# Optimization experiments

Measured on AMD Instinct MI355X. Metric: run time of the kernel, lower is better.

Reference implementation:

```python
import jax, jax.numpy as jnp
import numpy as np

B, S, H = 64, 2048, 512
NEG = -1e9

def setup_inputs() -> dict:
    key = jax.random.key(0)
    k1, k2, k3, k4, k5 = jax.random.split(key, 5)
    encoder_outputs = jax.random.normal(k1, (B, S, H), dtype=jnp.float32)
    mask = jax.random.randint(k2, (B, S), 0, 2).astype(bool)
    W = jax.random.normal(k3, (H, H), dtype=jnp.float32) / np.sqrt(H)
    b = jnp.zeros((H,), dtype=jnp.float32)
    v = jax.random.normal(k4, (H,), dtype=jnp.float32)  # context_vector
    return {"encoder_outputs": encoder_outputs, "mask": mask, "W": W, "b": b, "v": v}

def reference(encoder_outputs, mask, W, b, v):
    # u = tanh(x @ W^T + b): [B,S,H]
    u = jnp.tanh(jnp.einsum('bsh,oh->bso', encoder_outputs, W) + b)
    scores = jnp.einsum('bsh,h->bs', u, v)                 # [B,S]
    scores = jnp.where(mask, scores, NEG)
    attn_weights = jax.nn.softmax(scores, axis=1)          # [B,S]
    weighted_output = jnp.einsum('bsh,bs->bh', encoder_outputs, attn_weights)
    return weighted_output, attn_weights
```

## Files before the change

kernel.cpp:

```cpp
#include <hip/hip_runtime.h>
#include <hip/hip_fp16.h>
#include <stdint.h>

#define NEG_ (-1e9f)

typedef _Float16 f16x8 __attribute__((ext_vector_type(8)));
typedef float    f32x4 __attribute__((ext_vector_type(4)));

__device__ __forceinline__ float fast_tanh(float x) {
  float e = __expf(2.0f * x);
  return (e - 1.0f) * __builtin_amdgcn_rcpf(e + 1.0f);
}

__global__ __launch_bounds__(256) void k0_cvt_w(const float* __restrict__ W,
                                                __half* __restrict__ Wws) {
  int g = blockIdx.x * 256 + threadIdx.x;
  int lane = g & 63;
  int seg  = g >> 6;
  int io = seg & 3, ks = (seg >> 2) & 15, w = seg >> 6;
  int o = w * 64 + io * 16 + (lane & 15);
  int k = ks * 32 + (lane >> 4) * 8;
  const float2* src = (const float2*)(W + (size_t)o * 512 + k);
  __half2 h[4];
#pragma unroll
  for (int j = 0; j < 4; ++j) { float2 f = src[j]; h[j] = __floats2half2_rn(f.x, f.y); }
  uint4 u;
  u.x = *(uint32_t*)&h[0]; u.y = *(uint32_t*)&h[1];
  u.z = *(uint32_t*)&h[2]; u.w = *(uint32_t*)&h[3];
  *(uint4*)(Wws + (size_t)seg * 512 + (size_t)lane * 8) = u;
}

__global__ __launch_bounds__(512, 4) void k1_scores(
    const float* __restrict__ enc, const int* __restrict__ msk,
    const float* __restrict__ bias, const float* __restrict__ ctx,
    const __half* __restrict__ Wws, float* __restrict__ scores) {
  __shared__ __align__(16) __half Xl[64 * 512];

  const int t = threadIdx.x;
  const int w = t >> 6;
  const int lane = t & 63;
  const int quad = lane >> 4;
  const int l15 = lane & 15;
  const size_t mtile = blockIdx.x;

  {
    const float4* Xg = (const float4*)(enc + mtile * (size_t)(64 * 512));
#pragma unroll
    for (int j = 0; j < 8; ++j) {
      int g = j * 512 + t;
      int s = g >> 6, c = g & 63;
      float4 x0 = Xg[s * 128 + 2 * c];
      float4 x1 = Xg[s * 128 + 2 * c + 1];
      __half2 h0 = __floats2half2_rn(x0.x, x0.y);
      __half2 h1 = __floats2half2_rn(x0.z, x0.w);
      __half2 h2 = __floats2half2_rn(x1.x, x1.y);
      __half2 h3 = __floats2half2_rn(x1.z, x1.w);
      uint4 u;
      u.x = *(uint32_t*)&h0; u.y = *(uint32_t*)&h1;
      u.z = *(uint32_t*)&h2; u.w = *(uint32_t*)&h3;
      int pc = c ^ (s & 7);
      *(uint4*)&Xl[s * 512 + pc * 8] = u;
    }
  }
  __syncthreads();

  f16x8 abuf[3][4];
  auto aload = [&](int slot, int ks) {
    const f16x8* sp = (const f16x8*)(Wws +
        ((size_t)(w * 64 + ks * 4) * 512) + (size_t)lane * 8);
#pragma unroll
    for (int io = 0; io < 4; ++io) abuf[slot][io] = sp[io * 64];
  };
  aload(0, 0);
  aload(1, 1);

  f32x4 acc[4][4];
#pragma unroll
  for (int io = 0; io < 4; ++io)
#pragma unroll
    for (int is = 0; is < 4; ++is) acc[io][is] = (f32x4){0.f, 0.f, 0.f, 0.f};

#pragma unroll
  for (int ks = 0; ks < 16; ++ks) {
    if (ks + 2 < 16) aload((ks + 2) % 3, ks + 2);
    const f16x8* acur = abuf[ks % 3];
#pragma unroll
    for (int is = 0; is < 4; ++is) {
      int s = is * 16 + l15;
      const f16x8 bf = *(const f16x8*)&Xl[s * 512 + (((ks * 4 + quad) ^ (s & 7)) << 3)];
#pragma unroll
      for (int io = 0; io < 4; ++io)
        acc[io][is] = __builtin_amdgcn_mfma_f32_16x16x32_f16(acur[io], bf, acc[io][is], 0, 0, 0);
    }
  }

  float ps[4] = {0.f, 0.f, 0.f, 0.f};
#pragma unroll
  for (int io = 0; io < 4; ++io) {
    int ob = w * 64 + io * 16 + quad * 4;
    float4 b4 = *(const float4*)(bias + ob);
    float4 v4 = *(const float4*)(ctx + ob);
#pragma unroll
    for (int is = 0; is < 4; ++is) {
      const f32x4 a = acc[io][is];
      ps[is] += fast_tanh(a[0] + b4.x) * v4.x + fast_tanh(a[1] + b4.y) * v4.y +
                fast_tanh(a[2] + b4.z) * v4.z + fast_tanh(a[3] + b4.w) * v4.w;
    }
  }
#pragma unroll
  for (int is = 0; is < 4; ++is) {
    ps[is] += __shfl_xor(ps[is], 16, 64);
    ps[is] += __shfl_xor(ps[is], 32, 64);
  }

  __syncthreads();
  float* sred = (float*)&Xl[0];
  if (lane < 16) {
#pragma unroll
    for (int is = 0; is < 4; ++is) sred[w * 64 + is * 16 + lane] = ps[is];
  }
  __syncthreads();
  if (t < 64) {
    float sc = 0.f;
#pragma unroll
    for (int k = 0; k < 8; ++k) sc += sred[k * 64 + t];
    size_t row = mtile * 64 + t;
    scores[row] = msk[row] ? sc : NEG_;
  }
}

__global__ __launch_bounds__(256) void k2_softmax(float* __restrict__ attn) {
  const int b = blockIdx.x, t = threadIdx.x;
  float* row = attn + (size_t)b * 2048;
  float v[8];
  float mx = -3.4e38f;
#pragma unroll
  for (int i = 0; i < 8; ++i) { v[i] = row[t + 256 * i]; mx = fmaxf(mx, v[i]); }
#pragma unroll
  for (int off = 32; off >= 1; off >>= 1) mx = fmaxf(mx, __shfl_xor(mx, off, 64));
  __shared__ float r1[4], r2[4];
  int w = t >> 6, lane = t & 63;
  if (lane == 0) r1[w] = mx;
  __syncthreads();
  mx = fmaxf(fmaxf(r1[0], r1[1]), fmaxf(r1[2], r1[3]));
  float sum = 0.f;
#pragma unroll
  for (int i = 0; i < 8; ++i) { v[i] = __expf(v[i] - mx); sum += v[i]; }
#pragma unroll
  for (int off = 32; off >= 1; off >>= 1) sum += __shfl_xor(sum, off, 64);
  if (lane == 0) r2[w] = sum;
  __syncthreads();
  sum = r2[0] + r2[1] + r2[2] + r2[3];
  float inv = 1.0f / sum;
#pragma unroll
  for (int i = 0; i < 8; ++i) row[t + 256 * i] = v[i] * inv;
}

__global__ __launch_bounds__(256) void k3_wsum(const float* __restrict__ enc,
                                               const float* __restrict__ attn,
                                               float* __restrict__ out0) {
  const int bb = blockIdx.x >> 5, sc = blockIdx.x & 31, t = threadIdx.x;
  const int r = t >> 7;
  const int c = t & 127;
  __shared__ float a_s[64];
  __shared__ __align__(16) float4 part[128];
  if (t < 64) a_s[t] = attn[(size_t)bb * 2048 + sc * 64 + t];
  __syncthreads();
  const float4* Xg = (const float4*)(enc + ((size_t)bb * 2048 + (size_t)sc * 64) * 512);
  float4 acc = {0.f, 0.f, 0.f, 0.f};
#pragma unroll 8
  for (int s = r; s < 64; s += 2) {
    float a = a_s[s];
    float4 x = Xg[(size_t)s * 128 + c];
    acc.x = fmaf(a, x.x, acc.x);
    acc.y = fmaf(a, x.y, acc.y);
    acc.z = fmaf(a, x.z, acc.z);
    acc.w = fmaf(a, x.w, acc.w);
  }
  if (r) part[c] = acc;
  __syncthreads();
  if (!r) {
    float4 o = part[c];
    float* op = out0 + (size_t)bb * 512 + c * 4;
    atomicAdd(op + 0, acc.x + o.x);
    atomicAdd(op + 1, acc.y + o.y);
    atomicAdd(op + 2, acc.z + o.z);
    atomicAdd(op + 3, acc.w + o.w);
  }
}

extern "C" void kernel_launch(void* const* d_in, const int* in_sizes, int n_in,
                              void* d_out, int out_size, void* d_ws, size_t ws_size,
                              hipStream_t stream) {
  (void)in_sizes; (void)n_in; (void)out_size; (void)ws_size;
  const float* enc  = (const float*)d_in[0];
  const int*   msk  = (const int*)d_in[1];
  const float* W    = (const float*)d_in[2];
  const float* bias = (const float*)d_in[3];
  const float* ctx  = (const float*)d_in[4];
  float* out0 = (float*)d_out;
  float* attn = out0 + 64 * 512;
  __half* Wws = (__half*)d_ws;

  hipMemsetAsync(out0, 0, 64 * 512 * sizeof(float), stream);
  k0_cvt_w<<<128, 256, 0, stream>>>(W, Wws);
  k1_scores<<<2048, 512, 0, stream>>>(enc, msk, bias, ctx, Wws, attn);
  k2_softmax<<<64, 256, 0, stream>>>(attn);
  k3_wsum<<<2048, 256, 0, stream>>>(enc, attn, out0);
}
```

Baseline: 517.1 us.

## Fuse softmax-weighted sum into score kernel with online softmax partials

The score kernel now computes per-tile softmax partials (local max and sum) and, from the fp16 encoder tile already held in shared memory, a per-tile weighted partial sum. A small combine kernel rescales these partials to produce the final attention weights and output. This removes the second full read of the encoder tensor, the separate softmax pass and the atomic accumulation. In exchange it adds extra shared memory and a partial-sum workspace, and the weighted sum now uses fp16-rounded inputs, which may reduce accuracy.

```diff
diff --git a/kernel.cpp b/kernel.cpp
--- a/kernel.cpp
+++ b/kernel.cpp
@@ -33,8 +33,12 @@
 __global__ __launch_bounds__(512, 4) void k1_scores(
     const float* __restrict__ enc, const int* __restrict__ msk,
     const float* __restrict__ bias, const float* __restrict__ ctx,
-    const __half* __restrict__ Wws, float* __restrict__ scores) {
+    const __half* __restrict__ Wws, float* __restrict__ scores,
+    float* __restrict__ psum, float* __restrict__ mpart,
+    float* __restrict__ lpart) {
   __shared__ __align__(16) __half Xl[64 * 512];
+  __shared__ float sred[512];
+  __shared__ float pbuf[64];
 
   const int t = threadIdx.x;
   const int w = t >> 6;
@@ -114,7 +118,6 @@
   }
 
   __syncthreads();
-  float* sred = (float*)&Xl[0];
   if (lane < 16) {
 #pragma unroll
     for (int is = 0; is < 4; ++is) sred[w * 64 + is * 16 + lane] = ps[is];
@@ -125,67 +128,90 @@
 #pragma unroll
     for (int k = 0; k < 8; ++k) sc += sred[k * 64 + t];
     size_t row = mtile * 64 + t;
-    scores[row] = msk[row] ? sc : NEG_;
-  }
-}
-
-__global__ __launch_bounds__(256) void k2_softmax(float* __restrict__ attn) {
+    float sm = msk[row] ? sc : NEG_;
+    scores[row] = sm;
+    float m = sm;
+#pragma unroll
+    for (int off = 32; off >= 1; off >>= 1) m = fmaxf(m, __shfl_xor(m, off, 64));
+    float p = __expf(sm - m);
+    float l = p;
+#pragma unroll
+    for (int off = 32; off >= 1; off >>= 1) l += __shfl_xor(l, off, 64);
+    pbuf[t] = p;
+    if (t == 0) { mpart[mtile] = m; lpart[mtile] = l; }
+  }
+  __syncthreads();
+
+  float pacc[8] = {0.f, 0.f, 0.f, 0.f, 0.f, 0.f, 0.f, 0.f};
+  const int c = lane;
+#pragma unroll
+  for (int si = 0; si < 8; ++si) {
+    int s = (w << 3) + si;
+    float pv = pbuf[s];
+    f16x8 xv = *(const f16x8*)&Xl[s * 512 + ((c ^ (s & 7)) << 3)];
+#pragma unroll
+    for (int j = 0; j < 8; ++j) pacc[j] = fmaf(pv, (float)xv[j], pacc[j]);
+  }
+  __syncthreads();
+  float* pred = (float*)&Xl[0];
+  {
+    float4 lo = {pacc[0], pacc[1], pacc[2], pacc[3]};
+    float4 hi = {pacc[4], pacc[5], pacc[6], pacc[7]};
+    *(float4*)&pred[w * 512 + c * 4] = lo;
+    *(float4*)&pred[w * 512 + 256 + c * 4] = hi;
+  }
+  __syncthreads();
+  if (t < 128) {
+    int half = t & 1, c2 = t >> 1;
+    float4 a = {0.f, 0.f, 0.f, 0.f};
+#pragma unroll
+    for (int w2 = 0; w2 < 8; ++w2) {
+      float4 pv = *(const float4*)&pred[w2 * 512 + half * 256 + c2 * 4];
+      a.x += pv.x; a.y += pv.y; a.z += pv.z; a.w += pv.w;
+    }
+    *(float4*)&psum[mtile * 512 + (size_t)t * 4] = a;
+  }
+}
+
+__global__ __launch_bounds__(256) void k2_combine(
+    float* __restrict__ attn, const float* __restrict__ psum,
+    const float* __restrict__ mpart, const float* __restrict__ lpart,
+    float* __restrict__ out0) {
   const int b = blockIdx.x, t = threadIdx.x;
+  __shared__ float ml[32], ll[32];
+  if (t < 32) { ml[t] = mpart[b * 32 + t]; ll[t] = lpart[b * 32 + t]; }
+  __syncthreads();
+  float M = -3.4e38f;
+#pragma unroll
+  for (int i = 0; i < 32; ++i) M = fmaxf(M, ml[i]);
+  float wgt[32];
+  float Z = 0.f;
+#pragma unroll
+  for (int i = 0; i < 32; ++i) {
+    float e = __expf(ml[i] - M);
+    wgt[i] = e;
+    Z += e * ll[i];
+  }
+  float invZ = 1.0f / Z;
   float* row = attn + (size_t)b * 2048;
-  float v[8];
-  float mx = -3.4e38f;
-#pragma unroll
-  for (int i = 0; i < 8; ++i) { v[i] = row[t + 256 * i]; mx = fmaxf(mx, v[i]); }
-#pragma unroll
-  for (int off = 32; off >= 1; off >>= 1) mx = fmaxf(mx, __shfl_xor(mx, off, 64));
-  __shared__ float r1[4], r2[4];
-  int w = t >> 6, lane = t & 63;
-  if (lane == 0) r1[w] = mx;
-  __syncthreads();
-  mx = fmaxf(fmaxf(r1[0], r1[1]), fmaxf(r1[2], r1[3]));
-  float sum = 0.f;
-#pragma unroll
-  for (int i = 0; i < 8; ++i) { v[i] = __expf(v[i] - mx); sum += v[i]; }
-#pragma unroll
-  for (int off = 32; off >= 1; off >>= 1) sum += __shfl_xor(sum, off, 64);
-  if (lane == 0) r2[w] = sum;
-  __syncthreads();
-  sum = r2[0] + r2[1] + r2[2] + r2[3];
-  float inv = 1.0f / sum;
-#pragma unroll
-  for (int i = 0; i < 8; ++i) row[t + 256 * i] = v[i] * inv;
-}
-
-__global__ __launch_bounds__(256) void k3_wsum(const float* __restrict__ enc,
-                                               const float* __restrict__ attn,
-                                               float* __restrict__ out0) {
-  const int bb = blockIdx.x >> 5, sc = blockIdx.x & 31, t = threadIdx.x;
-  const int r = t >> 7;
-  const int c = t & 127;
-  __shared__ float a_s[64];
-  __shared__ __align__(16) float4 part[128];
-  if (t < 64) a_s[t] = attn[(size_t)bb * 2048 + sc * 64 + t];
-  __syncthreads();
-  const float4* Xg = (const float4*)(enc + ((size_t)bb * 2048 + (size_t)sc * 64) * 512);
-  float4 acc = {0.f, 0.f, 0.f, 0.f};
-#pragma unroll 8
-  for (int s = r; s < 64; s += 2) {
-    float a = a_s[s];
-    float4 x = Xg[(size_t)s * 128 + c];
-    acc.x = fmaf(a, x.x, acc.x);
-    acc.y = fmaf(a, x.y, acc.y);
-    acc.z = fmaf(a, x.z, acc.z);
-    acc.w = fmaf(a, x.w, acc.w);
-  }
-  if (r) part[c] = acc;
-  __syncthreads();
-  if (!r) {
-    float4 o = part[c];
-    float* op = out0 + (size_t)bb * 512 + c * 4;
-    atomicAdd(op + 0, acc.x + o.x);
-    atomicAdd(op + 1, acc.y + o.y);
-    atomicAdd(op + 2, acc.z + o.z);
-    atomicAdd(op + 3, acc.w + o.w);
+#pragma unroll
+  for (int i = 0; i < 8; ++i) {
+    int s = t + 256 * i;
+    row[s] = __expf(row[s] - M) * invZ;
+  }
+  if (t < 128) {
+    float4 a = {0.f, 0.f, 0.f, 0.f};
+#pragma unroll
+    for (int c2 = 0; c2 < 32; ++c2) {
+      float wv = wgt[c2];
+      float4 p = *(const float4*)&psum[((size_t)(b * 32 + c2)) * 512 + (size_t)t * 4];
+      a.x = fmaf(wv, p.x, a.x);
+      a.y = fmaf(wv, p.y, a.y);
+      a.z = fmaf(wv, p.z, a.z);
+      a.w = fmaf(wv, p.w, a.w);
+    }
+    float4 r = {a.x * invZ, a.y * invZ, a.z * invZ, a.w * invZ};
+    *(float4*)&out0[(size_t)b * 512 + (size_t)t * 4] = r;
   }
 }
 
@@ -200,11 +226,14 @@
   const float* ctx  = (const float*)d_in[4];
   float* out0 = (float*)d_out;
   float* attn = out0 + 64 * 512;
-  __half* Wws = (__half*)d_ws;
-
-  hipMemsetAsync(out0, 0, 64 * 512 * sizeof(float), stream);
+
+  __half* Wws  = (__half*)d_ws;
+  float*  psum = (float*)((char*)d_ws + (512u << 10));
+  float*  mprt = psum + (size_t)2048 * 512;
+  float*  lprt = mprt + 2048;
+
   k0_cvt_w<<<128, 256, 0, stream>>>(W, Wws);
-  k1_scores<<<2048, 512, 0, stream>>>(enc, msk, bias, ctx, Wws, attn);
-  k2_softmax<<<64, 256, 0, stream>>>(attn);
-  k3_wsum<<<2048, 256, 0, stream>>>(enc, attn, out0);
-}
+  k1_scores<<<2048, 512, 0, stream>>>(enc, msk, bias, ctx, Wws, attn,
+                                      psum, mprt, lprt);
+  k2_combine<<<64, 256, 0, stream>>>(attn, psum, mprt, lprt, out0);
+}
```

Measured after the change: 511.0 us. About the same (-1.2%).
